# Performance work log

Measured on AMD Instinct MI355X. Metric: run time of the kernel, lower is better.

## Reference

```python
import jax, jax.numpy as jnp
import numpy as np

N_NODES = 50000
N_EDGES = 800000
IN_F = 128
HID = 128
OUT = 2


def setup_inputs() -> dict:
    key = jax.random.key(0)
    ks = jax.random.split(key, 10)
    x = jax.random.normal(ks[0], (N_NODES, IN_F), dtype=jnp.float32)
    edge_index = jax.random.randint(ks[1], (2, N_EDGES), 0, N_NODES, dtype=jnp.int64)

    def lin(k, fan_in, fan_out):
        s = 1.0 / np.sqrt(fan_in)
        return jax.random.uniform(k, (fan_in, fan_out), jnp.float32, -s, s)

    return {
        "x": x,
        "edge_index": edge_index,
        # SAGEConv1: lin_l applied to mean-aggregated neighbors (with bias),
        # lin_r applied to root features (no bias), PyG convention.
        "W1_l": lin(ks[2], IN_F, HID),
        "W1_r": lin(ks[3], IN_F, HID),
        "b1": jnp.zeros((HID,), jnp.float32),
        "W2_l": lin(ks[4], HID, HID),
        "W2_r": lin(ks[5], HID, HID),
        "b2": jnp.zeros((HID,), jnp.float32),
        "Wfc": lin(ks[6], HID, OUT),
        "bfc": jnp.zeros((OUT,), jnp.float32),
    }


def reference(x, edge_index, W1_l, W1_r, b1, W2_l, W2_r, b2, Wfc, bfc):
    n = x.shape[0]
    src = edge_index[0]  # message source j
    dst = edge_index[1]  # aggregation target i
    # in-degree for mean aggregation (clamp to avoid div-by-zero for isolated nodes)
    deg = jax.ops.segment_sum(jnp.ones_like(dst, dtype=x.dtype), dst, num_segments=n)
    inv_deg = 1.0 / jnp.maximum(deg, 1.0)  # [n]

    def sage_conv(h, Wl, Wr, b):
        # mean over incoming neighbor features, then two linear maps
        agg = jax.ops.segment_sum(h[src], dst, num_segments=n) * inv_deg[:, None]
        return agg @ Wl + h @ Wr + b

    # dropout is identity at inference (training=False)
    h = jax.nn.relu(sage_conv(x, W1_l, W1_r, b1))
    h = jax.nn.relu(sage_conv(h, W2_l, W2_r, b2))
    return h @ Wfc + bfc  # [n, out] logits
```

## Files before the change

### kernel.cpp

```cpp
#include <hip/hip_runtime.h>

#define NN 50000
#define NE 800000
#define DEGCAP 64

#define NXCD 8
#define NPS ((NN + NXCD - 1) / NXCD)
#define SEPB 4096
#define NCHUNK ((NE + SEPB - 1) / SEPB)
#define SCAT_BLKS (NCHUNK * NXCD)
#define CVT_BLKS 6250
#define PREP_BLKS 32
#define K1_GRID (SCAT_BLKS + CVT_BLKS + PREP_BLKS + 1)

typedef short short8 __attribute__((ext_vector_type(8)));
typedef short short4v __attribute__((ext_vector_type(4)));
typedef float f32x4 __attribute__((ext_vector_type(4)));
typedef _Float16 half8v __attribute__((ext_vector_type(8)));

__device__ inline unsigned short f16_bits(float f) {
    _Float16 h = (_Float16)f;
    return __builtin_bit_cast(unsigned short, h);
}

__global__ __launch_bounds__(256) void k1_kernel(const float* __restrict__ x,
                                                 unsigned short* __restrict__ xb,
                                                 const float* __restrict__ W0,
                                                 const float* __restrict__ W1,
                                                 const float* __restrict__ W2,
                                                 const float* __restrict__ W3,
                                                 short* __restrict__ wf,
                                                 int* __restrict__ deg,
                                                 unsigned short* __restrict__ col,
                                                 const int* __restrict__ src,
                                                 const int* __restrict__ dst,
                                                 unsigned short* __restrict__ h1b) {
    int b = blockIdx.x;
    if (b < SCAT_BLKS) {
        int slot8 = b & 7;
        int chunk = b >> 3;
        int lo = slot8 * NPS, hi = lo + NPS;
        int base = chunk * SEPB;
        int end = base + SEPB;
        if (end > NE) end = NE;
        for (int i = base + (int)threadIdx.x; i < end; i += 256) {
            int d = dst[i];
            if (d >= lo && d < hi) {
                int s = src[i];
                int sl = atomicAdd(&deg[d], 1);
                col[((size_t)d << 6) + sl] = (unsigned short)s;
            }
        }
    } else if (b < SCAT_BLKS + CVT_BLKS) {
        int i = (b - SCAT_BLKS) * 256 + threadIdx.x;
        float4 v = ((const float4*)x)[i];
        short4v r;
        r[0] = (short)f16_bits(v.x);
        r[1] = (short)f16_bits(v.y);
        r[2] = (short)f16_bits(v.z);
        r[3] = (short)f16_bits(v.w);
        ((short4v*)xb)[i] = r;
    } else if (b < SCAT_BLKS + CVT_BLKS + PREP_BLKS) {
        int t = (b - SCAT_BLKS - CVT_BLKS) * 256 + threadIdx.x;
        int mat = t >> 11;
        const float* W = (mat == 0) ? W0 : (mat == 1) ? W1 : (mat == 2) ? W2 : W3;
        short* out = wf + (size_t)mat * 16384;
        int r = t & 2047;
        int nt = r >> 8;
        int kc = (r >> 6) & 3;
        int lane = r & 63;
        int n = nt * 16 + (lane & 15);
        int kbase = kc * 32 + ((lane >> 4) << 3);
        short8 vh;
#pragma unroll
        for (int j = 0; j < 8; ++j) {
            float w = W[(size_t)(kbase + j) * 128 + n];
            vh[j] = (short)f16_bits(w);
        }
        size_t o = ((size_t)((nt * 4 + kc) * 64 + lane)) * 8;
        *(short8*)(out + o) = vh;
    } else {
        int t = threadIdx.x;
        short8 z = {0, 0, 0, 0, 0, 0, 0, 0};
        if (t < 16) *(short8*)(xb + ((size_t)NN << 7) + (t << 3)) = z;
        else if (t < 32) *(short8*)(h1b + ((size_t)NN << 7) + ((t - 16) << 3)) = z;
    }
}

__global__ __launch_bounds__(256) void fused_sage(const unsigned short* __restrict__ hb,
                                                  const unsigned short* __restrict__ col,
                                                  const int* __restrict__ deg,
                                                  const short* __restrict__ Wf0,
                                                  const short* __restrict__ Wf1,
                                                  const float* __restrict__ bias,
                                                  unsigned short* __restrict__ outb,
                                                  const float* __restrict__ Wfc,
                                                  const float* __restrict__ bfc,
                                                  float* __restrict__ fcout,
                                                  int relu) {
    int lane = threadIdx.x & 63;
    int wave = threadIdx.x >> 6;
    int quad = lane >> 4, m16 = lane & 15;
    int row_base = blockIdx.x * 64 + wave * 16;
    int arow = row_base + m16;
    if (arow > NN - 1) arow = NN - 1;

    int dg = deg[arow];
    const unsigned short* cp = col + ((size_t)arow << 6);
    const unsigned short* tq = hb + (quad << 3);

    float accg[4][8];
#pragma unroll
    for (int kc = 0; kc < 4; ++kc)
#pragma unroll
        for (int j = 0; j < 8; ++j) accg[kc][j] = 0.f;

    int e = 0;
    for (; e + 4 <= dg; e += 4) {
        int c0 = cp[e], c1 = cp[e + 1], c2 = cp[e + 2], c3 = cp[e + 3];
        const unsigned short* r0 = tq + ((size_t)c0 << 7);
        const unsigned short* r1 = tq + ((size_t)c1 << 7);
        const unsigned short* r2 = tq + ((size_t)c2 << 7);
        const unsigned short* r3 = tq + ((size_t)c3 << 7);
#pragma unroll
        for (int kc = 0; kc < 4; ++kc) {
            half8v v0 = *(const half8v*)(r0 + kc * 32);
            half8v v1 = *(const half8v*)(r1 + kc * 32);
            half8v v2 = *(const half8v*)(r2 + kc * 32);
            half8v v3 = *(const half8v*)(r3 + kc * 32);
            half8v s = (v0 + v1) + (v2 + v3);
#pragma unroll
            for (int q = 0; q < 8; ++q) accg[kc][q] += (float)s[q];
        }
    }
    for (; e < dg; ++e) {
        const unsigned short* r0 = tq + ((size_t)cp[e] << 7);
#pragma unroll
        for (int kc = 0; kc < 4; ++kc) {
            half8v v0 = *(const half8v*)(r0 + kc * 32);
#pragma unroll
            for (int q = 0; q < 8; ++q) accg[kc][q] += (float)v0[q];
        }
    }

    float sdeg = 1.0f / (float)(dg > 0 ? dg : 1);
    half8v a0[4];
#pragma unroll
    for (int kc = 0; kc < 4; ++kc)
#pragma unroll
        for (int j = 0; j < 8; ++j) a0[kc][j] = (_Float16)(accg[kc][j] * sdeg);

    half8v a1[4];
#pragma unroll
    for (int kc = 0; kc < 4; ++kc)
        a1[kc] = *(const half8v*)(hb + ((size_t)arow << 7) + kc * 32 + (quad << 3));

    f32x4 acc[8];
#pragma unroll
    for (int nt = 0; nt < 8; ++nt) acc[nt] = (f32x4){0.f, 0.f, 0.f, 0.f};

#pragma unroll
    for (int kc = 0; kc < 4; ++kc) {
        const short* wp0 = Wf0 + ((size_t)kc * 64 + lane) * 8;
        const short* wp1 = Wf1 + ((size_t)kc * 64 + lane) * 8;
#pragma unroll
        for (int nt = 0; nt < 8; ++nt) {
            half8v b0 = *(const half8v*)(wp0 + (size_t)nt * 2048);
            half8v b1 = *(const half8v*)(wp1 + (size_t)nt * 2048);
            acc[nt] = __builtin_amdgcn_mfma_f32_16x16x32_f16(a0[kc], b0, acc[nt], 0, 0, 0);
            acc[nt] = __builtin_amdgcn_mfma_f32_16x16x32_f16(a1[kc], b1, acc[nt], 0, 0, 0);
        }
    }

    float bcol[8];
#pragma unroll
    for (int nt = 0; nt < 8; ++nt) bcol[nt] = bias[nt * 16 + m16];

    if (Wfc) {
        float w0[8], w1[8];
#pragma unroll
        for (int nt = 0; nt < 8; ++nt) {
            float2 wv = *(const float2*)(Wfc + 2 * (nt * 16 + m16));
            w0[nt] = wv.x;
            w1[nt] = wv.y;
        }
        float b0 = bfc[0], b1 = bfc[1];
#pragma unroll
        for (int r = 0; r < 4; ++r) {
            float p0 = 0.f, p1 = 0.f;
#pragma unroll
            for (int nt = 0; nt < 8; ++nt) {
                float v = fmaxf(acc[nt][r] + bcol[nt], 0.f);
                p0 += v * w0[nt];
                p1 += v * w1[nt];
            }
#pragma unroll
            for (int off = 1; off < 16; off <<= 1) {
                p0 += __shfl_xor(p0, off, 64);
                p1 += __shfl_xor(p1, off, 64);
            }
            int row = row_base + quad * 4 + r;
            if (m16 == 0 && row < NN) {
                float2 o;
                o.x = p0 + b0;
                o.y = p1 + b1;
                *(float2*)(fcout + 2 * (size_t)row) = o;
            }
        }
    } else {
#pragma unroll
        for (int r = 0; r < 4; ++r) {
            int row = row_base + quad * 4 + r;
            if (row >= NN) continue;
            unsigned short* opb = outb + ((size_t)row << 7) + m16;
#pragma unroll
            for (int nt = 0; nt < 8; ++nt) {
                float v = acc[nt][r] + bcol[nt];
                if (relu) v = fmaxf(v, 0.f);
                opb[nt * 16] = f16_bits(v);
            }
        }
    }
}

extern "C" void kernel_launch(void* const* d_in, const int* in_sizes, int n_in,
                              void* d_out, int out_size, void* d_ws, size_t ws_size,
                              hipStream_t stream) {
    const float* x   = (const float*)d_in[0];
    const int* edge  = (const int*)d_in[1];
    const float* W1l = (const float*)d_in[2];
    const float* W1r = (const float*)d_in[3];
    const float* b1  = (const float*)d_in[4];
    const float* W2l = (const float*)d_in[5];
    const float* W2r = (const float*)d_in[6];
    const float* b2  = (const float*)d_in[7];
    const float* Wfc = (const float*)d_in[8];
    const float* bfc = (const float*)d_in[9];
    float* out = (float*)d_out;

    const int* src = edge;
    const int* dst = edge + NE;

    char* ws = (char*)d_ws;
    size_t off = 0;
    auto alloc = [&](size_t bytes) -> char* {
        char* p = ws + off;
        off = (off + bytes + 511) & ~(size_t)511;
        return p;
    };
    int* deg              = (int*)alloc((size_t)NN * 4);
    short* wf             = (short*)alloc((size_t)4 * 16384 * 2);
    unsigned short* col   = (unsigned short*)alloc((size_t)NN * DEGCAP * 2);
    unsigned short* xb    = (unsigned short*)alloc((size_t)(NN + 1) * 128 * 2);
    unsigned short* h1b   = (unsigned short*)alloc((size_t)(NN + 1) * 128 * 2);
    (void)ws_size; (void)in_sizes; (void)n_in; (void)out_size;

    hipMemsetAsync(deg, 0, (size_t)NN * 4, stream);
    k1_kernel<<<K1_GRID, 256, 0, stream>>>(x, xb, W1l, W1r, W2l, W2r, wf,
                                           deg, col, src, dst, h1b);
    fused_sage<<<(NN + 63) / 64, 256, 0, stream>>>(xb, col, deg,
                                                   wf, wf + 16384, b1, h1b,
                                                   (const float*)0, (const float*)0,
                                                   (float*)0, 1);
    fused_sage<<<(NN + 63) / 64, 256, 0, stream>>>(h1b, col, deg,
                                                   wf + 2 * 16384, wf + 3 * 16384, b2,
                                                   (unsigned short*)0, Wfc, bfc, out, 0);
}
```

Before: 222.2 us.

## Gather neighbor rows with 16-lane groups per node and stage aggregates in LDS

Restructures neighbor aggregation so that each wave walks its 16 nodes in turn. The 64 lanes are split into 4 slots, each taking every fourth neighbor and loading 16-byte slices of a full 256-byte row, with partial sums reduced by cross-lane shuffles. The mean-aggregated f16 rows are written to shared memory and then read back as MFMA A-operands after a barrier. This aims to make gathers coalesced per row and to balance uneven degrees across lanes, at the cost of serialising over nodes, adding shuffles, LDS traffic and a block-wide sync.

```diff
diff --git a/kernel.cpp b/kernel.cpp
--- a/kernel.cpp
+++ b/kernel.cpp
@@ -87,7 +87,7 @@
     }
 }
 
-__global__ __launch_bounds__(256) void fused_sage(const unsigned short* __restrict__ hb,
+__global__ __launch_bounds__(256) void sage_layer(const unsigned short* __restrict__ hb,
                                                   const unsigned short* __restrict__ col,
                                                   const int* __restrict__ deg,
                                                   const short* __restrict__ Wf0,
@@ -98,62 +98,69 @@
                                                   const float* __restrict__ bfc,
                                                   float* __restrict__ fcout,
                                                   int relu) {
+    __shared__ unsigned short agg_s[64][136];
     int lane = threadIdx.x & 63;
-    int wave = threadIdx.x >> 6;
-    int quad = lane >> 4, m16 = lane & 15;
-    int row_base = blockIdx.x * 64 + wave * 16;
-    int arow = row_base + m16;
+    int wv = threadIdx.x >> 6;
+    int slot = lane >> 4, sub = lane & 15;
+    int row_base = blockIdx.x * 64;
+
+    const unsigned short* gbase = hb + (sub << 3);
+    for (int i = 0; i < 16; ++i) {
+        int li = wv * 16 + i;
+        int node = row_base + li;
+        if (node >= NN) {
+            if (slot == 0) {
+                short8 z = {0, 0, 0, 0, 0, 0, 0, 0};
+                *(short8*)&agg_s[li][sub << 3] = z;
+            }
+            continue;
+        }
+        int dg = deg[node];
+        const unsigned short* cp = col + ((size_t)node << 6);
+        float acc[8];
+#pragma unroll
+        for (int j = 0; j < 8; ++j) acc[j] = 0.f;
+        for (int e0 = slot; e0 < dg; e0 += 16) {
+            int c[4];
+#pragma unroll
+            for (int j = 0; j < 4; ++j) {
+                int e = e0 + 4 * j;
+                int cc = cp[e < DEGCAP ? e : 0];
+                c[j] = (e < dg) ? cc : NN;
+            }
+            half8v v[4];
+#pragma unroll
+            for (int j = 0; j < 4; ++j) v[j] = *(const half8v*)(gbase + ((size_t)c[j] << 7));
+            half8v s = (v[0] + v[1]) + (v[2] + v[3]);
+#pragma unroll
+            for (int q = 0; q < 8; ++q) acc[q] += (float)s[q];
+        }
+#pragma unroll
+        for (int j = 0; j < 8; ++j) {
+            acc[j] += __shfl_xor(acc[j], 16, 64);
+            acc[j] += __shfl_xor(acc[j], 32, 64);
+        }
+        if (slot == 0) {
+            float s = 1.0f / (float)(dg > 0 ? dg : 1);
+            short8 o;
+#pragma unroll
+            for (int j = 0; j < 8; ++j) o[j] = (short)f16_bits(acc[j] * s);
+            *(short8*)&agg_s[li][sub << 3] = o;
+        }
+    }
+    __syncthreads();
+
+    int quad = slot, m16 = sub;
+    int tb = row_base + wv * 16;
+    int arow = tb + m16;
     if (arow > NN - 1) arow = NN - 1;
 
-    int dg = deg[arow];
-    const unsigned short* cp = col + ((size_t)arow << 6);
-    const unsigned short* tq = hb + (quad << 3);
-
-    float accg[4][8];
-#pragma unroll
-    for (int kc = 0; kc < 4; ++kc)
-#pragma unroll
-        for (int j = 0; j < 8; ++j) accg[kc][j] = 0.f;
-
-    int e = 0;
-    for (; e + 4 <= dg; e += 4) {
-        int c0 = cp[e], c1 = cp[e + 1], c2 = cp[e + 2], c3 = cp[e + 3];
-        const unsigned short* r0 = tq + ((size_t)c0 << 7);
-        const unsigned short* r1 = tq + ((size_t)c1 << 7);
-        const unsigned short* r2 = tq + ((size_t)c2 << 7);
-        const unsigned short* r3 = tq + ((size_t)c3 << 7);
-#pragma unroll
-        for (int kc = 0; kc < 4; ++kc) {
-            half8v v0 = *(const half8v*)(r0 + kc * 32);
-            half8v v1 = *(const half8v*)(r1 + kc * 32);
-            half8v v2 = *(const half8v*)(r2 + kc * 32);
-            half8v v3 = *(const half8v*)(r3 + kc * 32);
-            half8v s = (v0 + v1) + (v2 + v3);
-#pragma unroll
-            for (int q = 0; q < 8; ++q) accg[kc][q] += (float)s[q];
-        }
-    }
-    for (; e < dg; ++e) {
-        const unsigned short* r0 = tq + ((size_t)cp[e] << 7);
-#pragma unroll
-        for (int kc = 0; kc < 4; ++kc) {
-            half8v v0 = *(const half8v*)(r0 + kc * 32);
-#pragma unroll
-            for (int q = 0; q < 8; ++q) accg[kc][q] += (float)v0[q];
-        }
-    }
-
-    float sdeg = 1.0f / (float)(dg > 0 ? dg : 1);
-    half8v a0[4];
-#pragma unroll
-    for (int kc = 0; kc < 4; ++kc)
-#pragma unroll
-        for (int j = 0; j < 8; ++j) a0[kc][j] = (_Float16)(accg[kc][j] * sdeg);
-
-    half8v a1[4];
-#pragma unroll
-    for (int kc = 0; kc < 4; ++kc)
+    half8v a0[4], a1[4];
+#pragma unroll
+    for (int kc = 0; kc < 4; ++kc) {
+        a0[kc] = *(const half8v*)&agg_s[wv * 16 + m16][kc * 32 + (quad << 3)];
         a1[kc] = *(const half8v*)(hb + ((size_t)arow << 7) + kc * 32 + (quad << 3));
+    }
 
     f32x4 acc[8];
 #pragma unroll
@@ -180,9 +187,9 @@
         float w0[8], w1[8];
 #pragma unroll
         for (int nt = 0; nt < 8; ++nt) {
-            float2 wv = *(const float2*)(Wfc + 2 * (nt * 16 + m16));
-            w0[nt] = wv.x;
-            w1[nt] = wv.y;
+            float2 wv2 = *(const float2*)(Wfc + 2 * (nt * 16 + m16));
+            w0[nt] = wv2.x;
+            w1[nt] = wv2.y;
         }
         float b0 = bfc[0], b1 = bfc[1];
 #pragma unroll
@@ -199,7 +206,7 @@
                 p0 += __shfl_xor(p0, off, 64);
                 p1 += __shfl_xor(p1, off, 64);
             }
-            int row = row_base + quad * 4 + r;
+            int row = tb + quad * 4 + r;
             if (m16 == 0 && row < NN) {
                 float2 o;
                 o.x = p0 + b0;
@@ -210,7 +217,7 @@
     } else {
 #pragma unroll
         for (int r = 0; r < 4; ++r) {
-            int row = row_base + quad * 4 + r;
+            int row = tb + quad * 4 + r;
             if (row >= NN) continue;
             unsigned short* opb = outb + ((size_t)row << 7) + m16;
 #pragma unroll
@@ -258,11 +265,11 @@
     hipMemsetAsync(deg, 0, (size_t)NN * 4, stream);
     k1_kernel<<<K1_GRID, 256, 0, stream>>>(x, xb, W1l, W1r, W2l, W2r, wf,
                                            deg, col, src, dst, h1b);
-    fused_sage<<<(NN + 63) / 64, 256, 0, stream>>>(xb, col, deg,
+    sage_layer<<<(NN + 63) / 64, 256, 0, stream>>>(xb, col, deg,
                                                    wf, wf + 16384, b1, h1b,
                                                    (const float*)0, (const float*)0,
                                                    (float*)0, 1);
-    fused_sage<<<(NN + 63) / 64, 256, 0, stream>>>(h1b, col, deg,
+    sage_layer<<<(NN + 63) / 64, 256, 0, stream>>>(h1b, col, deg,
                                                    wf + 2 * 16384, wf + 3 * 16384, b2,
                                                    (unsigned short*)0, Wfc, bfc, out, 0);
 }
```

Measured after the change: 253.8 us. 14.2% more time.
